# Performance work log

Measured on AMD Instinct MI355X. Metric: run time of the kernel, lower is better.

The kernel has to match this reference:

```python
import jax, jax.numpy as jnp
import numpy as np

N_NODES = 50000
N_EDGES = 500000
HIDDEN = 128
HEADS = 8
HEAD_DIM = HIDDEN // HEADS
EPS = 1e-16  # PyG softmax denominator epsilon


def _kaiming(key, shape):
    fan_in = shape[0]
    return jax.random.normal(key, shape, dtype=jnp.float32) * np.sqrt(2.0 / fan_in)


def prelu(x, a):
    return jnp.maximum(x, 0.0) + a * jnp.minimum(x, 0.0)


def transformer_conv(x, src, dst, Wq, bq, Wk, bk, Wv, bv, Ws, bs):
    """PyG TransformerConv (concat=True, root_weight=True, beta=False), eval mode."""
    N = x.shape[0]
    q = (x @ Wq + bq).reshape(N, HEADS, HEAD_DIM)
    k = (x @ Wk + bk).reshape(N, HEADS, HEAD_DIM)
    v = (x @ Wv + bv).reshape(N, HEADS, HEAD_DIM)
    # per-edge attention: query from destination, key/value from source
    score = jnp.einsum('ehd,ehd->eh', q[dst], k[src]) / np.sqrt(HEAD_DIM)  # [E,H]
    m = jax.ops.segment_max(score, dst, num_segments=N)                     # [N,H]
    e = jnp.exp(score - m[dst])
    s = jax.ops.segment_sum(e, dst, num_segments=N)
    alpha = e / (s[dst] + EPS)                                              # [E,H]
    agg = jax.ops.segment_sum(alpha[..., None] * v[src], dst, num_segments=N)
    return agg.reshape(N, HIDDEN) + x @ Ws + bs  # skip connection (lin_skip)


def setup_inputs() -> dict:
    key = jax.random.key(0)
    ks = jax.random.split(key, 12)
    inp = {
        'x': jax.random.normal(ks[0], (N_NODES, HIDDEN), dtype=jnp.float32),
        'edge_index': jax.random.randint(ks[1], (2, N_EDGES), 0, N_NODES, dtype=jnp.int64 if jax.config.jax_enable_x64 else jnp.int32),
        'prelu_w': jnp.full((1,), 0.25, dtype=jnp.float32),
    }
    i = 2
    for layer in (1, 2):
        for nm in ('q', 'k', 'v', 's'):
            inp[f'W{nm}{layer}'] = _kaiming(ks[i], (HIDDEN, HIDDEN))
            inp[f'b{nm}{layer}'] = jnp.zeros((HIDDEN,), dtype=jnp.float32)
            i += 1
        ks = jax.random.split(ks[-1], 12)
        i = 0
    return inp


def reference(x, edge_index, prelu_w,
              Wq1, bq1, Wk1, bk1, Wv1, bv1, Ws1, bs1,
              Wq2, bq2, Wk2, bk2, Wv2, bv2, Ws2, bs2):
    src, dst = edge_index[0], edge_index[1]
    o = transformer_conv(x, src, dst, Wq1, bq1, Wk1, bk1, Wv1, bv1, Ws1, bs1)
    o = prelu(o, prelu_w)
    o = transformer_conv(o, src, dst, Wq2, bq2, Wk2, bk2, Wv2, bv2, Ws2, bs2)
    o = o + x  # residual
    return prelu(o, prelu_w)
```

## Files before the change

kernel.cpp:

```cpp
#include <hip/hip_runtime.h>

#define NN 50000
#define NE 500000
#define HID 128
#define MT4 3128
#define MT4_PER_XCD 391
#define HISTB 1954
#define SCAN_B 196
#define CSRB 256

typedef __attribute__((ext_vector_type(8))) short short8;
typedef __attribute__((ext_vector_type(8))) _Float16 half8;
typedef __attribute__((ext_vector_type(2))) _Float16 half2v;
typedef __attribute__((ext_vector_type(4))) float f32x4;
typedef unsigned short ushort_t;
typedef unsigned int uint32;
typedef _Float16 half_t;

__device__ __forceinline__ ushort_t f2h(float f) {
    union { half_t h; ushort_t u; } x; x.h = (half_t)f; return x.u;
}
__device__ __forceinline__ half2v u2h2(uint32 u) {
    union { uint32 u; half2v h; } x; x.u = u; return x.h;
}

__global__ __launch_bounds__(256) void prep(
    const float* __restrict__ Wq1, const float* __restrict__ Wk1,
    const float* __restrict__ Wv1, const float* __restrict__ Ws1,
    const float* __restrict__ Wq2, const float* __restrict__ Wk2,
    const float* __restrict__ Wv2, const float* __restrict__ Ws2,
    ushort_t* __restrict__ Bt1, ushort_t* __restrict__ Bt2,
    int* __restrict__ counts, int* __restrict__ bars)
{
    int b = blockIdx.x, t = threadIdx.x;
    if (b < 512) {
        int idx = b * 256 + t;
        int layer = idx >> 16;
        int r = idx & 65535;
        int col = r >> 7;
        int kk = r & 127;
        int wsel = col >> 7;
        const float* W = (layer == 0)
            ? ((wsel == 0) ? Wq1 : (wsel == 1) ? Wk1 : (wsel == 2) ? Wv1 : Ws1)
            : ((wsel == 0) ? Wq2 : (wsel == 1) ? Wk2 : (wsel == 2) ? Wv2 : Ws2);
        float val = W[kk * HID + (col & 127)];
        if (wsel == 0) val *= 0.25f;
        (layer == 0 ? Bt1 : Bt2)[r] = f2h(val);
    } else if (b < 512 + SCAN_B) {
        int i = (b - 512) * 256 + t;
        if (i < NN) counts[i] = 0;
    } else {
        if (t < 8) bars[t] = 0;
    }
}

template <int LAYER>
__device__ __forceinline__ void gemm_body(
    ushort_t* As, ushort_t* Bs, int wgid,
    const float* __restrict__ Xf, const ushort_t* __restrict__ Xh,
    const ushort_t* __restrict__ Bt,
    const float* __restrict__ bqp, const float* __restrict__ bkp,
    const float* __restrict__ bvp, const float* __restrict__ bsp,
    ushort_t* __restrict__ Qb, ushort_t* __restrict__ KVb, ushort_t* __restrict__ Sfb)
{
    const int xcd = wgid & 7, kidx = wgid >> 3;
    const int local = xcd * MT4_PER_XCD + kidx;
    const int mtile = local >> 2;
    const int g = local & 3;
    const int Mbase = mtile * 64;
    const int tid = threadIdx.x;
    const int lane = tid & 63, wave = tid >> 6;

    #pragma unroll
    for (int it = 0; it < 4; ++it) {
        int lin = it * 256 + tid;
        int row = lin >> 4, s = lin & 15;
        int rg = Mbase + row; if (rg >= NN) rg = NN - 1;
        short8 v;
        if (LAYER == 1) {
            float4 f0 = *reinterpret_cast<const float4*>(Xf + (size_t)rg * HID + s * 8);
            float4 f1 = *reinterpret_cast<const float4*>(Xf + (size_t)rg * HID + s * 8 + 4);
            v[0] = (short)f2h(f0.x); v[1] = (short)f2h(f0.y);
            v[2] = (short)f2h(f0.z); v[3] = (short)f2h(f0.w);
            v[4] = (short)f2h(f1.x); v[5] = (short)f2h(f1.y);
            v[6] = (short)f2h(f1.z); v[7] = (short)f2h(f1.w);
        } else {
            v = *reinterpret_cast<const short8*>(Xh + (size_t)rg * HID + s * 8);
        }
        *reinterpret_cast<short8*>((char*)As + row * 256 + ((s * 16) ^ ((row & 7) * 16))) = v;
    }
    #pragma unroll
    for (int it = 0; it < 8; ++it) {
        int lin = it * 256 + tid;
        int col = lin >> 4, s = lin & 15;
        short8 v = *reinterpret_cast<const short8*>(
            Bt + (size_t)(g * 128 + col) * HID + s * 8);
        *reinterpret_cast<short8*>((char*)Bs + col * 256 + ((s * 16) ^ ((col & 7) * 16))) = v;
    }
    __syncthreads();

    const int l15 = lane & 15;
    const int wrow = wave * 16;
    f32x4 acc[8] = {};
    #pragma unroll
    for (int kk = 0; kk < 4; ++kk) {
        int kbyte = kk * 64 + (lane >> 4) * 16;
        int ar = wrow + l15;
        half8 a = *reinterpret_cast<const half8*>(
            (const char*)As + ar * 256 + (kbyte ^ ((ar & 7) * 16)));
        #pragma unroll
        for (int nb = 0; nb < 8; ++nb) {
            int c = nb * 16 + l15;
            half8 b = *reinterpret_cast<const half8*>(
                (const char*)Bs + c * 256 + (kbyte ^ ((c & 7) * 16)));
            acc[nb] = __builtin_amdgcn_mfma_f32_16x16x32_f16(a, b, acc[nb], 0, 0, 0);
        }
    }
    __syncthreads();

    const float* bias = (g == 0) ? bqp : (g == 1) ? bkp : (g == 2) ? bvp : bsp;
    float* Cs = reinterpret_cast<float*>(Bs);
    #pragma unroll
    for (int nb = 0; nb < 8; ++nb) {
        int c = nb * 16 + l15;
        float bb = bias[c];
        if (g == 0) bb *= 0.25f;
        #pragma unroll
        for (int r = 0; r < 4; ++r) {
            int rl = wrow + (lane >> 4) * 4 + r;
            Cs[rl * 128 + c] = acc[nb][r] + bb;
        }
    }
    __syncthreads();

    #pragma unroll
    for (int it = 0; it < 4; ++it) {
        int lin = it * 256 + tid;
        int row = lin >> 4, s = lin & 15;
        int rg = Mbase + row;
        if (rg < NN) {
            float4 v0 = *reinterpret_cast<float4*>(&Cs[row * 128 + s * 8]);
            float4 v1 = *reinterpret_cast<float4*>(&Cs[row * 128 + s * 8 + 4]);
            short8 o;
            o[0] = (short)f2h(v0.x); o[1] = (short)f2h(v0.y);
            o[2] = (short)f2h(v0.z); o[3] = (short)f2h(v0.w);
            o[4] = (short)f2h(v1.x); o[5] = (short)f2h(v1.y);
            o[6] = (short)f2h(v1.z); o[7] = (short)f2h(v1.w);
            ushort_t* dst = (g == 0) ? (Qb  + (size_t)rg * HID + s * 8)
                          : (g == 1) ? (KVb + (size_t)rg * 256 + s * 8)
                          : (g == 2) ? (KVb + (size_t)rg * 256 + 128 + s * 8)
                          :            (Sfb + (size_t)rg * HID + s * 8);
            *reinterpret_cast<short8*>(dst) = o;
        }
    }
}

__global__ __launch_bounds__(256) void gemm1_hist(
    const float* __restrict__ Xf, const ushort_t* __restrict__ Bt,
    const float* __restrict__ bqp, const float* __restrict__ bkp,
    const float* __restrict__ bvp, const float* __restrict__ bsp,
    ushort_t* __restrict__ Qb, ushort_t* __restrict__ KVb, ushort_t* __restrict__ Sfb,
    const int* __restrict__ dstIdx, int* __restrict__ counts)
{
    __shared__ ushort_t As[64 * 128];
    __shared__ ushort_t Bs[128 * 128];
    if (blockIdx.x < MT4) {
        gemm_body<1>(As, Bs, blockIdx.x, Xf, nullptr, Bt,
                     bqp, bkp, bvp, bsp, Qb, KVb, Sfb);
    } else {
        int e = (blockIdx.x - MT4) * 256 + threadIdx.x;
        if (e < NE) atomicAdd(&counts[dstIdx[e]], 1);
    }
}

__global__ __launch_bounds__(256) void gemm2(
    const ushort_t* __restrict__ Xh, const ushort_t* __restrict__ Bt,
    const float* __restrict__ bqp, const float* __restrict__ bkp,
    const float* __restrict__ bvp, const float* __restrict__ bsp,
    ushort_t* __restrict__ Qb, ushort_t* __restrict__ KVb, ushort_t* __restrict__ Sfb)
{
    __shared__ ushort_t As[64 * 128];
    __shared__ ushort_t Bs[128 * 128];
    gemm_body<2>(As, Bs, blockIdx.x, nullptr, Xh, Bt,
                 bqp, bkp, bvp, bsp, Qb, KVb, Sfb);
}

__device__ __forceinline__ void grid_barrier(int* ctr)
{
    __syncthreads();
    if (threadIdx.x == 0) {
        __threadfence();
        atomicAdd(ctr, 1);
        while (__hip_atomic_load(ctr, __ATOMIC_RELAXED, __HIP_MEMORY_SCOPE_AGENT) < CSRB)
            __builtin_amdgcn_s_sleep(2);
        __threadfence();
    }
    __syncthreads();
}

__global__ __launch_bounds__(256) void csr_build(
    const int* __restrict__ src, const int* __restrict__ dst,
    const int* __restrict__ counts, int* __restrict__ bsum, int* __restrict__ bbase,
    int* __restrict__ offsets, int* __restrict__ cursor, int* __restrict__ csr_src,
    int* __restrict__ bars)
{
    __shared__ int sh[256];
    __shared__ int ws[4];
    const int t = threadIdx.x, b = blockIdx.x;

    if (b < SCAN_B) {
        int i = b * 256 + t;
        int v = (i < NN) ? counts[i] : 0;
        #pragma unroll
        for (int o = 1; o < 64; o <<= 1) v += __shfl_xor(v, o);
        if ((t & 63) == 0) ws[t >> 6] = v;
        __syncthreads();
        if (t == 0) bsum[b] = ws[0] + ws[1] + ws[2] + ws[3];
    }
    grid_barrier(bars + 0);

    if (b == 0) {
        int v = (t < SCAN_B) ? bsum[t] : 0;
        sh[t] = v;
        __syncthreads();
        for (int o = 1; o < 256; o <<= 1) {
            int u = (t >= o) ? sh[t - o] : 0;
            __syncthreads();
            sh[t] += u;
            __syncthreads();
        }
        if (t < SCAN_B) bbase[t] = (t > 0) ? sh[t - 1] : 0;
    }
    grid_barrier(bars + 1);

    if (b < SCAN_B) {
        int i = b * 256 + t;
        int v = (i < NN) ? counts[i] : 0;
        sh[t] = v;
        __syncthreads();
        for (int o = 1; o < 256; o <<= 1) {
            int u = (t >= o) ? sh[t - o] : 0;
            __syncthreads();
            sh[t] += u;
            __syncthreads();
        }
        int excl = sh[t] - v + bbase[b];
        if (i < NN) { offsets[i] = excl; cursor[i] = excl; }
        if (i == NN - 1) offsets[NN] = excl + v;
    }
    grid_barrier(bars + 2);

    for (int e = b * 256 + t; e < NE; e += CSRB * 256) {
        int pos = atomicAdd(&cursor[dst[e]], 1);
        csr_src[pos] = src[e];
    }
}

template <int LAYER>
__global__ __launch_bounds__(256) void edge_aggregate(
    const half_t* __restrict__ Qh, const half_t* __restrict__ KVh,
    const half_t* __restrict__ Sh,
    const int* __restrict__ offsets, const int* __restrict__ csr_src,
    const float* __restrict__ xres, const float* __restrict__ prelu_w,
    float* __restrict__ outF, ushort_t* __restrict__ outH)
{
    const int lane = threadIdx.x & 63;
    const int wid  = __builtin_amdgcn_readfirstlane((int)(threadIdx.x >> 6));
    const int node = blockIdx.x * 4 + wid;
    const bool hi  = lane >= 32;
    const int  c   = lane & 31;

    uint2 qu = *reinterpret_cast<const uint2*>(Qh + (size_t)node * HID + c * 4);
    half2v qa = u2h2(qu.x), qb = u2h2(qu.y);
    const float q0 = (float)qa[0], q1 = (float)qa[1];
    const float q2 = (float)qb[0], q3 = (float)qb[1];

    const int beg = offsets[node];
    const int end = offsets[node + 1];

    float den = 0.f, a0 = 0.f, a1 = 0.f, a2 = 0.f, a3 = 0.f;

#define COMPUTE(KU, VU) {                                                      \
        half2v k01 = u2h2((KU).x), k23 = u2h2((KU).y);                         \
        float p = (float)k01[0] * q0 + (float)k01[1] * q1                      \
                + (float)k23[0] * q2 + (float)k23[1] * q3;                     \
        p += __shfl_xor(p, 1); p += __shfl_xor(p, 2);                          \
        float w = __expf(p);                                                   \
        den += w;                                                              \
        half2v v01 = u2h2((VU).x), v23 = u2h2((VU).y);                         \
        a0 += w * (float)v01[0]; a1 += w * (float)v01[1];                      \
        a2 += w * (float)v23[0]; a3 += w * (float)v23[1]; }

    int i = beg;
    for (; i + 8 <= end; i += 8) {
        uint2 ku[4], vu[4];
        #pragma unroll
        for (int j = 0; j < 4; ++j) {
            int s = hi ? csr_src[i + 2 * j + 1] : csr_src[i + 2 * j];
            const half_t* kv = KVh + (size_t)s * 256 + c * 4;
            ku[j] = *reinterpret_cast<const uint2*>(kv);
            vu[j] = *reinterpret_cast<const uint2*>(kv + 128);
        }
        #pragma unroll
        for (int j = 0; j < 4; ++j) COMPUTE(ku[j], vu[j])
    }
    for (; i + 2 <= end; i += 2) {
        int s = hi ? csr_src[i + 1] : csr_src[i];
        const half_t* kv = KVh + (size_t)s * 256 + c * 4;
        uint2 ku = *reinterpret_cast<const uint2*>(kv);
        uint2 vu = *reinterpret_cast<const uint2*>(kv + 128);
        COMPUTE(ku, vu)
    }
    if (i < end) {
        int s = csr_src[i];
        const half_t* kv = KVh + (size_t)s * 256 + c * 4;
        uint2 ku = *reinterpret_cast<const uint2*>(kv);
        uint2 vu = *reinterpret_cast<const uint2*>(kv + 128);
        half2v k01 = u2h2(ku.x), k23 = u2h2(ku.y);
        float p = (float)k01[0] * q0 + (float)k01[1] * q1
                + (float)k23[0] * q2 + (float)k23[1] * q3;
        p += __shfl_xor(p, 1); p += __shfl_xor(p, 2);
        float w = hi ? 0.f : __expf(p);
        den += w;
        half2v v01 = u2h2(vu.x), v23 = u2h2(vu.y);
        a0 += w * (float)v01[0]; a1 += w * (float)v01[1];
        a2 += w * (float)v23[0]; a3 += w * (float)v23[1];
    }
#undef COMPUTE

    den += __shfl_xor(den, 32);
    a0 += __shfl_xor(a0, 32); a1 += __shfl_xor(a1, 32);
    a2 += __shfl_xor(a2, 32); a3 += __shfl_xor(a3, 32);

    if (!hi) {
        float inv = (den > 0.f) ? 1.f / den : 0.f;
        uint2 su = *reinterpret_cast<const uint2*>(Sh + (size_t)node * HID + c * 4);
        half2v s01 = u2h2(su.x), s23 = u2h2(su.y);
        float r0 = a0 * inv + (float)s01[0];
        float r1 = a1 * inv + (float)s01[1];
        float r2 = a2 * inv + (float)s23[0];
        float r3 = a3 * inv + (float)s23[1];
        if (LAYER == 2) {
            float4 xr = *reinterpret_cast<const float4*>(xres + (size_t)node * HID + c * 4);
            r0 += xr.x; r1 += xr.y; r2 += xr.z; r3 += xr.w;
        }
        const float al = prelu_w[0];
        r0 = fmaxf(r0, 0.f) + al * fminf(r0, 0.f);
        r1 = fmaxf(r1, 0.f) + al * fminf(r1, 0.f);
        r2 = fmaxf(r2, 0.f) + al * fminf(r2, 0.f);
        r3 = fmaxf(r3, 0.f) + al * fminf(r3, 0.f);
        if (LAYER == 1) {
            uint2 o;
            o.x = (uint32)f2h(r0) | ((uint32)f2h(r1) << 16);
            o.y = (uint32)f2h(r2) | ((uint32)f2h(r3) << 16);
            *reinterpret_cast<uint2*>(outH + (size_t)node * HID + c * 4) = o;
        } else {
            float4 o; o.x = r0; o.y = r1; o.z = r2; o.w = r3;
            *reinterpret_cast<float4*>(outF + (size_t)node * HID + c * 4) = o;
        }
    }
}

extern "C" void kernel_launch(void* const* d_in, const int* in_sizes, int n_in,
                              void* d_out, int out_size, void* d_ws, size_t ws_size,
                              hipStream_t stream)
{
    const float* x       = (const float*)d_in[0];
    const int*   ei      = (const int*)d_in[1];
    const float* prelu_w = (const float*)d_in[2];
    const float* Wq1 = (const float*)d_in[3],  *bq1 = (const float*)d_in[4];
    const float* Wk1 = (const float*)d_in[5],  *bk1 = (const float*)d_in[6];
    const float* Wv1 = (const float*)d_in[7],  *bv1 = (const float*)d_in[8];
    const float* Ws1 = (const float*)d_in[9],  *bs1 = (const float*)d_in[10];
    const float* Wq2 = (const float*)d_in[11], *bq2 = (const float*)d_in[12];
    const float* Wk2 = (const float*)d_in[13], *bk2 = (const float*)d_in[14];
    const float* Wv2 = (const float*)d_in[15], *bv2 = (const float*)d_in[16];
    const float* Ws2 = (const float*)d_in[17], *bs2 = (const float*)d_in[18];

    char* w = (char*)d_ws;
    size_t off = 0;
    auto alloc = [&](size_t bytes) { void* p = w + off; off += (bytes + 255) & ~(size_t)255; return p; };
    ushort_t* x1h  = (ushort_t*)alloc((size_t)NN * HID * 2);
    ushort_t* Qb   = (ushort_t*)alloc((size_t)NN * HID * 2);
    ushort_t* KVb  = (ushort_t*)alloc((size_t)NN * 256 * 2);
    ushort_t* Sfb  = (ushort_t*)alloc((size_t)NN * HID * 2);
    ushort_t* Bt1  = (ushort_t*)alloc((size_t)512 * 128 * 2);
    ushort_t* Bt2  = (ushort_t*)alloc((size_t)512 * 128 * 2);
    int* counts  = (int*)alloc(NN * sizeof(int));
    int* bsum    = (int*)alloc(256 * sizeof(int));
    int* bbase   = (int*)alloc(256 * sizeof(int));
    int* offsets = (int*)alloc((NN + 1) * sizeof(int));
    int* cursor  = (int*)alloc(NN * sizeof(int));
    int* csr_src = (int*)alloc(NE * sizeof(int));
    int* bars    = (int*)alloc(8 * sizeof(int));
    (void)ws_size; (void)in_sizes; (void)n_in; (void)out_size;

    const int* srcIdx = ei;
    const int* dstIdx = ei + NE;

    prep<<<512 + SCAN_B + 1, 256, 0, stream>>>(Wq1, Wk1, Wv1, Ws1,
                                               Wq2, Wk2, Wv2, Ws2,
                                               Bt1, Bt2, counts, bars);
    gemm1_hist<<<MT4 + HISTB, 256, 0, stream>>>(x, Bt1, bq1, bk1, bv1, bs1,
                                                Qb, KVb, Sfb, dstIdx, counts);
    csr_build<<<CSRB, 256, 0, stream>>>(srcIdx, dstIdx, counts, bsum, bbase,
                                        offsets, cursor, csr_src, bars);
    edge_aggregate<1><<<NN / 4, 256, 0, stream>>>((const half_t*)Qb, (const half_t*)KVb,
                                                  (const half_t*)Sfb, offsets, csr_src,
                                                  nullptr, prelu_w, nullptr, x1h);
    gemm2<<<MT4, 256, 0, stream>>>(x1h, Bt2, bq2, bk2, bv2, bs2, Qb, KVb, Sfb);
    edge_aggregate<2><<<NN / 4, 256, 0, stream>>>((const half_t*)Qb, (const half_t*)KVb,
                                                  (const half_t*)Sfb, offsets, csr_src,
                                                  x, prelu_w, (float*)d_out, nullptr);
}
```

Baseline: 240.9 us.

## Replace grid-barrier CSR build with atomic-base scan and separate scatter kernel

The single CSR build kernel, which relied on three software grid barriers, is split in two. A one-pass block scan takes each block's base offset from a global atomic counter, and a separate fully parallel kernel scatters the edges. Because the atomic assigns bases in arbitrary block order, segments are no longer globally sorted by node, so the aggregate kernels now take each segment's end from offset plus count. This removes barrier spinning and the extra scan pass, at the cost of one more kernel launch and a less ordered CSR layout.

Measured after the change: 195.0 us. -19.0%, faster.

```diff
diff --git a/kernel.cpp b/kernel.cpp
--- a/kernel.cpp
+++ b/kernel.cpp
@@ -7,7 +7,6 @@
 #define MT4_PER_XCD 391
 #define HISTB 1954
 #define SCAN_B 196
-#define CSRB 256
 
 typedef __attribute__((ext_vector_type(8))) short short8;
 typedef __attribute__((ext_vector_type(8))) _Float16 half8;
@@ -30,7 +29,7 @@
     const float* __restrict__ Wq2, const float* __restrict__ Wk2,
     const float* __restrict__ Wv2, const float* __restrict__ Ws2,
     ushort_t* __restrict__ Bt1, ushort_t* __restrict__ Bt2,
-    int* __restrict__ counts, int* __restrict__ bars)
+    int* __restrict__ counts, int* __restrict__ gcursor)
 {
     int b = blockIdx.x, t = threadIdx.x;
     if (b < 512) {
@@ -50,7 +49,7 @@
         int i = (b - 512) * 256 + t;
         if (i < NN) counts[i] = 0;
     } else {
-        if (t < 8) bars[t] = 0;
+        if (t == 0) *gcursor = 0;
     }
 }
 
@@ -185,72 +184,34 @@
                  bqp, bkp, bvp, bsp, Qb, KVb, Sfb);
 }
 
-__device__ __forceinline__ void grid_barrier(int* ctr)
-{
-    __syncthreads();
-    if (threadIdx.x == 0) {
-        __threadfence();
-        atomicAdd(ctr, 1);
-        while (__hip_atomic_load(ctr, __ATOMIC_RELAXED, __HIP_MEMORY_SCOPE_AGENT) < CSRB)
-            __builtin_amdgcn_s_sleep(2);
-        __threadfence();
-    }
-    __syncthreads();
-}
-
-__global__ __launch_bounds__(256) void csr_build(
-    const int* __restrict__ src, const int* __restrict__ dst,
-    const int* __restrict__ counts, int* __restrict__ bsum, int* __restrict__ bbase,
-    int* __restrict__ offsets, int* __restrict__ cursor, int* __restrict__ csr_src,
-    int* __restrict__ bars)
+__global__ __launch_bounds__(256) void scan_fused(
+    const int* __restrict__ counts, int* __restrict__ gcursor,
+    int* __restrict__ offsets, int* __restrict__ cursor)
 {
     __shared__ int sh[256];
-    __shared__ int ws[4];
-    const int t = threadIdx.x, b = blockIdx.x;
-
-    if (b < SCAN_B) {
-        int i = b * 256 + t;
-        int v = (i < NN) ? counts[i] : 0;
-        #pragma unroll
-        for (int o = 1; o < 64; o <<= 1) v += __shfl_xor(v, o);
-        if ((t & 63) == 0) ws[t >> 6] = v;
+    __shared__ int base_sh;
+    const int t = threadIdx.x;
+    const int i = blockIdx.x * 256 + t;
+    int v = (i < NN) ? counts[i] : 0;
+    sh[t] = v;
+    __syncthreads();
+    for (int o = 1; o < 256; o <<= 1) {
+        int u = (t >= o) ? sh[t - o] : 0;
         __syncthreads();
-        if (t == 0) bsum[b] = ws[0] + ws[1] + ws[2] + ws[3];
-    }
-    grid_barrier(bars + 0);
-
-    if (b == 0) {
-        int v = (t < SCAN_B) ? bsum[t] : 0;
-        sh[t] = v;
+        sh[t] += u;
         __syncthreads();
-        for (int o = 1; o < 256; o <<= 1) {
-            int u = (t >= o) ? sh[t - o] : 0;
-            __syncthreads();
-            sh[t] += u;
-            __syncthreads();
-        }
-        if (t < SCAN_B) bbase[t] = (t > 0) ? sh[t - 1] : 0;
-    }
-    grid_barrier(bars + 1);
-
-    if (b < SCAN_B) {
-        int i = b * 256 + t;
-        int v = (i < NN) ? counts[i] : 0;
-        sh[t] = v;
-        __syncthreads();
-        for (int o = 1; o < 256; o <<= 1) {
-            int u = (t >= o) ? sh[t - o] : 0;
-            __syncthreads();
-            sh[t] += u;
-            __syncthreads();
-        }
-        int excl = sh[t] - v + bbase[b];
-        if (i < NN) { offsets[i] = excl; cursor[i] = excl; }
-        if (i == NN - 1) offsets[NN] = excl + v;
-    }
-    grid_barrier(bars + 2);
-
-    for (int e = b * 256 + t; e < NE; e += CSRB * 256) {
+    }
+    if (t == 255) base_sh = atomicAdd(gcursor, sh[255]);
+    __syncthreads();
+    int excl = sh[t] - v + base_sh;
+    if (i < NN) { offsets[i] = excl; cursor[i] = excl; }
+}
+
+__global__ void scatter_kernel(const int* __restrict__ src, const int* __restrict__ dst,
+                               int* __restrict__ cursor, int* __restrict__ csr_src)
+{
+    int e = blockIdx.x * blockDim.x + threadIdx.x;
+    if (e < NE) {
         int pos = atomicAdd(&cursor[dst[e]], 1);
         csr_src[pos] = src[e];
     }
@@ -260,7 +221,8 @@
 __global__ __launch_bounds__(256) void edge_aggregate(
     const half_t* __restrict__ Qh, const half_t* __restrict__ KVh,
     const half_t* __restrict__ Sh,
-    const int* __restrict__ offsets, const int* __restrict__ csr_src,
+    const int* __restrict__ offsets, const int* __restrict__ counts,
+    const int* __restrict__ csr_src,
     const float* __restrict__ xres, const float* __restrict__ prelu_w,
     float* __restrict__ outF, ushort_t* __restrict__ outH)
 {
@@ -276,7 +238,7 @@
     const float q2 = (float)qb[0], q3 = (float)qb[1];
 
     const int beg = offsets[node];
-    const int end = offsets[node + 1];
+    const int end = beg + counts[node];
 
     float den = 0.f, a0 = 0.f, a1 = 0.f, a2 = 0.f, a3 = 0.f;
 
@@ -387,12 +349,10 @@
     ushort_t* Bt1  = (ushort_t*)alloc((size_t)512 * 128 * 2);
     ushort_t* Bt2  = (ushort_t*)alloc((size_t)512 * 128 * 2);
     int* counts  = (int*)alloc(NN * sizeof(int));
-    int* bsum    = (int*)alloc(256 * sizeof(int));
-    int* bbase   = (int*)alloc(256 * sizeof(int));
-    int* offsets = (int*)alloc((NN + 1) * sizeof(int));
+    int* offsets = (int*)alloc(NN * sizeof(int));
     int* cursor  = (int*)alloc(NN * sizeof(int));
     int* csr_src = (int*)alloc(NE * sizeof(int));
-    int* bars    = (int*)alloc(8 * sizeof(int));
+    int* gcursor = (int*)alloc(256);
     (void)ws_size; (void)in_sizes; (void)n_in; (void)out_size;
 
     const int* srcIdx = ei;
@@ -400,16 +360,16 @@
 
     prep<<<512 + SCAN_B + 1, 256, 0, stream>>>(Wq1, Wk1, Wv1, Ws1,
                                                Wq2, Wk2, Wv2, Ws2,
-                                               Bt1, Bt2, counts, bars);
+                                               Bt1, Bt2, counts, gcursor);
     gemm1_hist<<<MT4 + HISTB, 256, 0, stream>>>(x, Bt1, bq1, bk1, bv1, bs1,
                                                 Qb, KVb, Sfb, dstIdx, counts);
-    csr_build<<<CSRB, 256, 0, stream>>>(srcIdx, dstIdx, counts, bsum, bbase,
-                                        offsets, cursor, csr_src, bars);
+    scan_fused<<<SCAN_B, 256, 0, stream>>>(counts, gcursor, offsets, cursor);
+    scatter_kernel<<<(NE + 255) / 256, 256, 0, stream>>>(srcIdx, dstIdx, cursor, csr_src);
     edge_aggregate<1><<<NN / 4, 256, 0, stream>>>((const half_t*)Qb, (const half_t*)KVb,
-                                                  (const half_t*)Sfb, offsets, csr_src,
+                                                  (const half_t*)Sfb, offsets, counts, csr_src,
                                                   nullptr, prelu_w, nullptr, x1h);
     gemm2<<<MT4, 256, 0, stream>>>(x1h, Bt2, bq2, bk2, bv2, bs2, Qb, KVb, Sfb);
     edge_aggregate<2><<<NN / 4, 256, 0, stream>>>((const half_t*)Qb, (const half_t*)KVb,
-                                                  (const half_t*)Sfb, offsets, csr_src,
+                                                  (const half_t*)Sfb, offsets, counts, csr_src,
                                                   x, prelu_w, (float*)d_out, nullptr);
 }
```
